# Performance work log

Hardware: AMD Instinct MI355X
Metric: run time of the kernel (lower is better)

## Reference

```python
import jax, jax.numpy as jnp
import numpy as np

PATCH = 256
CH = 28


def setup_inputs() -> dict:
    key = jax.random.key(0)
    kx, km = jax.random.split(key)
    x = jax.random.normal(kx, (32, PATCH, PATCH, CH), dtype=jnp.float32)
    # bk: binary mask from a (P/2, P/2) random pattern, tiled 2x2, repeated over channels
    ms = PATCH // 2
    bk_fixed = jnp.round(jax.random.uniform(km, (ms, ms), dtype=jnp.float32))
    bk_tile = jnp.tile(bk_fixed, (2, 2))                      # [P, P]
    bk = jnp.repeat(bk_tile[:, :, None], CH, axis=2)          # [P, P, C]
    return {"x": x, "bk": bk}


def reference(x, bk):
    # Original math per channel ch:
    #   y[i,j,ch] = x[(i+ch)%P, j, ch] * bk[i,j,ch]      (roll by -ch, multiply)
    #   z[i,j,ch] = y[(i-ch)%P, j, ch]                   (roll back by +ch)
    # => z[i,j,ch] = x[i,j,ch] * bk[(i-ch)%P, j, ch]
    # So fuse the two rolls into a single per-channel roll of the mask,
    # then a fused multiply + channel-sum (single memory pass).
    C = x.shape[-1]
    shifts = jnp.arange(C)
    # roll each channel of the mask by +ch along height
    bk_shifted = jax.vmap(lambda m, s: jnp.roll(m, s, axis=0),
                          in_axes=(2, 0), out_axes=2)(bk, shifts)  # [P, P, C]
    # fused shift-multiply-accumulate: [B, P, P]
    return jnp.sum(x * bk_shifted[None], axis=-1)
```

## Files before the change

### kernel.cpp

```cpp
#include <hip/hip_runtime.h>

#define P 256
#define C 28
#define NPIX (P * P)
#define MASK_ELEMS (P * P * C)

__global__ __launch_bounds__(256) void prep_mask_kernel(
    const float* __restrict__ bk, float* __restrict__ bks) {
    int idx = blockIdx.x * 256 + threadIdx.x;
    if (idx >= MASK_ELEMS) return;
    int ch = idx % C;
    int ij = idx / C;
    int j = ij & (P - 1);
    int i = ij >> 8;
    int src_row = (i - ch) & (P - 1);
    bks[idx] = bk[(src_row * P + j) * C + ch];
}

__global__ __launch_bounds__(256) void codednet_main_kernel(
    const float* __restrict__ x, const float* __restrict__ bks,
    float* __restrict__ out) {
    int pid = blockIdx.x * 256 + threadIdx.x;
    int pix = pid & (NPIX - 1);
    const float4* xp = reinterpret_cast<const float4*>(x + (size_t)pid * C);
    const float4* mp = reinterpret_cast<const float4*>(bks + (size_t)pix * C);
    float acc = 0.f;
#pragma unroll
    for (int k = 0; k < 7; ++k) {
        float4 a = xp[k];
        float4 m = mp[k];
        acc += a.x * m.x + a.y * m.y + a.z * m.z + a.w * m.w;
    }
    out[pid] = acc;
}

__global__ __launch_bounds__(256) void codednet_inline_kernel(
    const float* __restrict__ x, const float* __restrict__ bk,
    float* __restrict__ out) {
    int pid = blockIdx.x * 256 + threadIdx.x;
    int pix = pid & (NPIX - 1);
    int j = pix & (P - 1);
    int i = pix >> 8;
    const float* xp = x + (size_t)pid * C;
    float acc = 0.f;
#pragma unroll
    for (int ch = 0; ch < C; ++ch) {
        int src_row = (i - ch) & (P - 1);
        acc += xp[ch] * bk[(src_row * P + j) * C + ch];
    }
    out[pid] = acc;
}

extern "C" void kernel_launch(void* const* d_in, const int* in_sizes, int n_in,
                              void* d_out, int out_size, void* d_ws, size_t ws_size,
                              hipStream_t stream) {
    const float* x  = (const float*)d_in[0];
    const float* bk = (const float*)d_in[1];
    float* out = (float*)d_out;

    const int total = out_size;
    const int nblocks = (total + 255) / 256;

    if (ws_size >= (size_t)MASK_ELEMS * sizeof(float)) {
        float* bks = (float*)d_ws;
        prep_mask_kernel<<<(MASK_ELEMS + 255) / 256, 256, 0, stream>>>(bk, bks);
        codednet_main_kernel<<<nblocks, 256, 0, stream>>>(x, bks, out);
    } else {
        codednet_inline_kernel<<<nblocks, 256, 0, stream>>>(x, bk, out);
    }
}
```

Measured before the change: 327.1 us.

## Coalesce float4 loads across threads and reduce per-pixel partials in shared memory

The main kernel now assigns one float4 of the input to each thread, so consecutive threads read consecutive 16-byte chunks instead of each thread striding 112 bytes through its own pixel. Partial dot products go to shared memory and 64 threads each sum 7 partials per pixel. Blocks are 448 threads covering 64 pixels. This targets uncoalesced global loads on a memory-bound reduction, at the cost of a barrier, shared-memory traffic, and only 64 of 448 threads doing the final sums and stores.

Result: no change. 321.5 us (-1.7%).

```diff
diff --git a/kernel.cpp b/kernel.cpp
--- a/kernel.cpp
+++ b/kernel.cpp
@@ -3,7 +3,11 @@
 #define P 256
 #define C 28
 #define NPIX (P * P)
-#define MASK_ELEMS (P * P * C)
+#define MASK_ELEMS (NPIX * C)
+#define Q 7
+#define BLK 448
+#define PIX_PER_BLK 64
+#define BLKS_PER_IMG 1024
 
 __global__ __launch_bounds__(256) void prep_mask_kernel(
     const float* __restrict__ bk, float* __restrict__ bks) {
@@ -17,21 +21,22 @@
     bks[idx] = bk[(src_row * P + j) * C + ch];
 }
 
-__global__ __launch_bounds__(256) void codednet_main_kernel(
-    const float* __restrict__ x, const float* __restrict__ bks,
+__global__ __launch_bounds__(BLK) void codednet_f4_kernel(
+    const float4* __restrict__ x4, const float4* __restrict__ m4,
     float* __restrict__ out) {
-    int pid = blockIdx.x * 256 + threadIdx.x;
-    int pix = pid & (NPIX - 1);
-    const float4* xp = reinterpret_cast<const float4*>(x + (size_t)pid * C);
-    const float4* mp = reinterpret_cast<const float4*>(bks + (size_t)pix * C);
-    float acc = 0.f;
-#pragma unroll
-    for (int k = 0; k < 7; ++k) {
-        float4 a = xp[k];
-        float4 m = mp[k];
-        acc += a.x * m.x + a.y * m.y + a.z * m.z + a.w * m.w;
+    __shared__ float s[BLK];
+    int t = threadIdx.x;
+    int f = blockIdx.x * BLK + t;
+    int mf = (blockIdx.x & (BLKS_PER_IMG - 1)) * BLK + t;
+    float4 a = x4[f];
+    float4 m = m4[mf];
+    s[t] = a.x * m.x + a.y * m.y + a.z * m.z + a.w * m.w;
+    __syncthreads();
+    if (t < PIX_PER_BLK) {
+        const float* p = s + t * Q;
+        float acc = ((p[0] + p[1]) + (p[2] + p[3])) + ((p[4] + p[5]) + p[6]);
+        out[blockIdx.x * PIX_PER_BLK + t] = acc;
     }
-    out[pid] = acc;
 }
 
 __global__ __launch_bounds__(256) void codednet_inline_kernel(
@@ -59,13 +64,14 @@
     float* out = (float*)d_out;
 
     const int total = out_size;
-    const int nblocks = (total + 255) / 256;
 
     if (ws_size >= (size_t)MASK_ELEMS * sizeof(float)) {
         float* bks = (float*)d_ws;
         prep_mask_kernel<<<(MASK_ELEMS + 255) / 256, 256, 0, stream>>>(bk, bks);
-        codednet_main_kernel<<<nblocks, 256, 0, stream>>>(x, bks, out);
+        const int nblocks = total / PIX_PER_BLK;
+        codednet_f4_kernel<<<nblocks, BLK, 0, stream>>>(
+            (const float4*)x, (const float4*)bks, out);
     } else {
-        codednet_inline_kernel<<<nblocks, 256, 0, stream>>>(x, bk, out);
+        codednet_inline_kernel<<<(total + 255) / 256, 256, 0, stream>>>(x, bk, out);
     }
 }
```
